# Performance work log

Measured on AMD Instinct MI355X. Metric: run time of the kernel, lower is better.

Reference implementation:

```python
import jax, jax.numpy as jnp
import numpy as np
import math

NUM_HEADS = 12
HEAD_DIM = 64
DEGREE = 3
POLY_DIM = HEAD_DIM * (DEGREE + 1)  # 256
MEM_HID = 512
HIDDEN = 768


def setup_inputs() -> dict:
    key = jax.random.key(0)
    ks = jax.random.split(key, 6)
    B, S = 4, 2048
    hidden_states = jax.random.normal(ks[0], (B, S, HIDDEN), dtype=jnp.float32)
    # q projection weight stored (in, out) so y = x @ Wq
    Wq = jax.random.normal(ks[1], (HIDDEN, HIDDEN), dtype=jnp.float32) / np.sqrt(HIDDEN)
    # polynomial coefficients initialized to 1/i!
    coeffs = jnp.array([1.0 / math.factorial(i) for i in range(DEGREE + 1)], dtype=jnp.float32)
    # deep memory MLP: Linear(poly_dim->mem_hid) + ReLU + Linear(mem_hid->poly_dim)
    W1 = jax.random.normal(ks[2], (POLY_DIM, MEM_HID), dtype=jnp.float32) / np.sqrt(POLY_DIM)
    b1 = jnp.zeros((MEM_HID,), dtype=jnp.float32)
    W2 = jax.random.normal(ks[3], (MEM_HID, POLY_DIM), dtype=jnp.float32) / np.sqrt(MEM_HID)
    b2 = jnp.zeros((POLY_DIM,), dtype=jnp.float32)
    return {"hidden_states": hidden_states, "Wq": Wq, "coeffs": coeffs,
            "W1": W1, "b1": b1, "W2": W2, "b2": b2}


def _poly_map(x, coeffs):
    # x: [..., head_dim] -> [..., head_dim*(degree+1)]
    xs = jnp.clip(x, -10.0, 10.0)
    feats = [coeffs[0] * jnp.ones_like(x)]
    for i in range(1, DEGREE + 1):
        feats.append(jnp.clip(coeffs[i] * xs ** i, -1e6, 1e6))
    return jnp.concatenate(feats, axis=-1)


def reference(hidden_states, Wq, coeffs, W1, b1, W2, b2):
    B, S, H = hidden_states.shape
    # q projection -> [B, S, nh, hd]
    q = (hidden_states @ Wq).reshape(B, S, NUM_HEADS, HEAD_DIM)
    # polynomial feature expansion -> [B, S, nh, poly_dim]
    poly_q = _poly_map(q, coeffs)
    flat = poly_q.reshape(-1, POLY_DIM)  # [B*S*nh, poly_dim]
    # deep memory MLP (test-time memory read)
    h = jax.nn.relu(flat @ W1 + b1)
    mem = h @ W2 + b2  # [B*S*nh, poly_dim]
    # slice first head_dim dims, fold heads back into hidden
    out = mem[:, :HEAD_DIM].reshape(B, S, NUM_HEADS * HEAD_DIM)
    return out
```

## Files before the change

### kernel.cpp

```cpp
#include <hip/hip_runtime.h>


typedef unsigned short u16;
typedef __attribute__((ext_vector_type(8))) short short8;
typedef __attribute__((ext_vector_type(4))) float f32x4;
typedef __attribute__((ext_vector_type(4))) u16 u16x4;

__device__ __forceinline__ u16 f2bf(float f) {
    unsigned u = __builtin_bit_cast(unsigned, f);
    u += 0x7FFFu + ((u >> 16) & 1u);
    return (u16)(u >> 16);
}

__device__ __forceinline__ unsigned cvtpk_bf16(float lo, float hi) {
    unsigned r;
    asm("v_cvt_pk_bf16_f32 %0, %1, %2" : "=v"(r) : "v"(lo), "v"(hi));
    return r;
}

__device__ __forceinline__ void gl2lds16(const void* g, void* l) {
    __builtin_amdgcn_global_load_lds(
        (const __attribute__((address_space(1))) unsigned int*)g,
        (__attribute__((address_space(3))) unsigned int*)l, 16, 0, 0);
}


__global__ __launch_bounds__(256) void cast_f32_bf16(const float* __restrict__ in,
                                                     u16* __restrict__ out, int n4) {
    int i = blockIdx.x * 256 + threadIdx.x;
    if (i < n4) {
        float4 v = reinterpret_cast<const float4*>(in)[i];
        u16x4 o = {f2bf(v.x), f2bf(v.y), f2bf(v.z), f2bf(v.w)};
        reinterpret_cast<u16x4*>(out)[i] = o;
    }
}

__global__ __launch_bounds__(256) void transpose_cast(const float* __restrict__ in,
                                                      u16* __restrict__ out,
                                                      int R, int Cin) {
    __shared__ float t[32][33];
    const int c0 = blockIdx.x * 32, r0 = blockIdx.y * 32;
    const int tx = threadIdx.x, ty = threadIdx.y;
    #pragma unroll
    for (int j = 0; j < 32; j += 8)
        t[ty + j][tx] = in[(size_t)(r0 + ty + j) * Cin + c0 + tx];
    __syncthreads();
    #pragma unroll
    for (int j = 0; j < 32; j += 8)
        out[(size_t)(c0 + ty + j) * R + r0 + tx] = f2bf(t[tx][ty + j]);
}

__global__ __launch_bounds__(256) void make_b1eff(const float* __restrict__ W1,
                                                  const float* __restrict__ b1,
                                                  const float* __restrict__ coeffs,
                                                  float* __restrict__ b1e) {
    const int n = blockIdx.x * 256 + threadIdx.x;
    float s = 0.f;
    #pragma unroll 8
    for (int k = 0; k < 64; ++k) s += W1[k * 512 + n];
    b1e[n] = b1[n] + coeffs[0] * s;
}


__global__ __launch_bounds__(256)
void gemm1_poly(const u16* __restrict__ A, const u16* __restrict__ B,
                const float* __restrict__ coeffs, u16* __restrict__ P)
{
    __shared__ u16 As[128 * 32];
    __shared__ u16 Bs[128 * 32];

    const int tid = threadIdx.x;
    const int w = tid >> 6, lane = tid & 63;
    const int lrow = lane >> 2, lslot = lane & 3;
    const int m16 = lane & 15, quad = lane >> 4;
    const int bm = blockIdx.x * 128, bn = blockIdx.y * 128;
    const int wr = (w & 1) * 64, wc = (w >> 1) * 64;

    const float c1 = coeffs[1], c2 = coeffs[2], c3 = coeffs[3];

    f32x4 acc[4][4];
    #pragma unroll
    for (int i = 0; i < 4; ++i)
        #pragma unroll
        for (int j = 0; j < 4; ++j)
            acc[i][j] = (f32x4){0.f, 0.f, 0.f, 0.f};

    for (int k0 = 0; k0 < 768; k0 += 32) {
        #pragma unroll
        for (int i = 0; i < 2; ++i) {
            const int row = (w * 2 + i) * 16 + lrow;
            const int cc = lslot ^ ((row >> 2) & 3);
            gl2lds16(A + (size_t)(bm + row) * 768 + k0 + cc * 8, &As[row * 32 + lslot * 8]);
            gl2lds16(B + (size_t)(bn + row) * 768 + k0 + cc * 8, &Bs[row * 32 + lslot * 8]);
        }
        __syncthreads();

        short8 af[4], bf[4];
        #pragma unroll
        for (int i = 0; i < 4; ++i) {
            const int row = wr + i * 16 + m16;
            const int s = quad ^ ((row >> 2) & 3);
            af[i] = *reinterpret_cast<const short8*>(&As[row * 32 + s * 8]);
        }
        #pragma unroll
        for (int j = 0; j < 4; ++j) {
            const int row = wc + j * 16 + m16;
            const int s = quad ^ ((row >> 2) & 3);
            bf[j] = *reinterpret_cast<const short8*>(&Bs[row * 32 + s * 8]);
        }
        #pragma unroll
        for (int i = 0; i < 4; ++i)
            #pragma unroll
            for (int j = 0; j < 4; ++j)
                acc[i][j] = __builtin_amdgcn_mfma_f32_16x16x32_bf16(af[i], bf[j], acc[i][j], 0, 0, 0);
        __syncthreads();
    }

    #pragma unroll
    for (int j = 0; j < 4; ++j) {
        const int col = bn + wc + j * 16 + m16;
        const int h = col >> 6, d = col & 63;
        #pragma unroll
        for (int i = 0; i < 4; ++i) {
            #pragma unroll
            for (int r = 0; r < 4; ++r) {
                const int row = bm + wr + i * 16 + quad * 4 + r;
                u16* pp = P + ((size_t)row * 12 + h) * 192 + d;
                float x = fminf(fmaxf(acc[i][j][r], -10.f), 10.f);
                const float x2 = x * x;
                const unsigned p12 = cvtpk_bf16(c1 * x, c2 * x2);
                const unsigned p3  = cvtpk_bf16(c3 * x2 * x, 0.f);
                pp[0]   = (u16)p12;
                pp[64]  = (u16)(p12 >> 16);
                pp[128] = (u16)p3;
            }
        }
    }
}

__global__ __launch_bounds__(256)
void gemm23(const u16* __restrict__ P, const u16* __restrict__ W1t,
            const float* __restrict__ b1e, const u16* __restrict__ W2t,
            const float* __restrict__ b2, float* __restrict__ out)
{
    __shared__ u16 As[128 * 32];
    __shared__ u16 Bs[128 * 32];
    __shared__ u16 Hs[4][128 * 32];

    const int tid = threadIdx.x;
    const int w = tid >> 6, lane = tid & 63;
    const int lrow = lane >> 2, lslot = lane & 3;
    const int m16 = lane & 15, quad = lane >> 4;
    const size_t r0 = (size_t)blockIdx.x * 128;
    const int w0 = w & 1, w1 = w >> 1;

    f32x4 accO[4][2];
    #pragma unroll
    for (int i = 0; i < 4; ++i)
        #pragma unroll
        for (int j = 0; j < 2; ++j)
            accO[i][j] = (f32x4){0.f, 0.f, 0.f, 0.f};

    #pragma unroll 1
    for (int s = 0; s < 4; ++s) {
        f32x4 accH[4][4];
        #pragma unroll
        for (int i = 0; i < 4; ++i)
            #pragma unroll
            for (int j = 0; j < 4; ++j)
                accH[i][j] = (f32x4){0.f, 0.f, 0.f, 0.f};

        for (int c = 0; c < 6; ++c) {
            #pragma unroll
            for (int i = 0; i < 2; ++i) {
                const int row = (w * 2 + i) * 16 + lrow;
                const int cc = lslot ^ ((row >> 2) & 3);
                gl2lds16(W1t + (size_t)(s * 128 + row) * 256 + 64 + c * 32 + cc * 8,
                         &As[row * 32 + lslot * 8]);
                gl2lds16(P + (r0 + row) * 192 + c * 32 + cc * 8,
                         &Bs[row * 32 + lslot * 8]);
            }
            __syncthreads();

            short8 af[4], bf[4];
            #pragma unroll
            for (int i = 0; i < 4; ++i) {
                const int row = w0 * 64 + i * 16 + m16;
                const int ss = quad ^ ((row >> 2) & 3);
                af[i] = *reinterpret_cast<const short8*>(&As[row * 32 + ss * 8]);
            }
            #pragma unroll
            for (int j = 0; j < 4; ++j) {
                const int row = w1 * 64 + j * 16 + m16;
                const int ss = quad ^ ((row >> 2) & 3);
                bf[j] = *reinterpret_cast<const short8*>(&Bs[row * 32 + ss * 8]);
            }
            #pragma unroll
            for (int i = 0; i < 4; ++i)
                #pragma unroll
                for (int j = 0; j < 4; ++j)
                    accH[i][j] = __builtin_amdgcn_mfma_f32_16x16x32_bf16(af[i], bf[j], accH[i][j], 0, 0, 0);
            __syncthreads();
        }

        #pragma unroll
        for (int i = 0; i < 4; ++i) {
            const int lb = w0 * 64 + i * 16 + quad * 4;
            const f32x4 bv = *reinterpret_cast<const f32x4*>(&b1e[s * 128 + lb]);
            const int hc = lb >> 5;
            #pragma unroll
            for (int j = 0; j < 4; ++j) {
                const int tc = w1 * 64 + j * 16 + m16;
                const float h0 = fmaxf(accH[i][j][0] + bv[0], 0.f);
                const float h1 = fmaxf(accH[i][j][1] + bv[1], 0.f);
                const float h2 = fmaxf(accH[i][j][2] + bv[2], 0.f);
                const float h3 = fmaxf(accH[i][j][3] + bv[3], 0.f);
                uint2 v;
                v.x = cvtpk_bf16(h0, h1);
                v.y = cvtpk_bf16(h2, h3);
                const int sl = ((lb >> 3) & 3) ^ ((tc >> 2) & 3);
                *reinterpret_cast<uint2*>(&Hs[hc][tc * 32 + sl * 8 + (lb & 7)]) = v;
            }
        }

        {
            u16* dst = (w < 2) ? As : Bs;
            #pragma unroll
            for (int i = 0; i < 4; ++i) {
                const int row = i * 16 + lrow;
                const int cc = lslot ^ ((row >> 2) & 3);
                gl2lds16(W2t + (size_t)row * 512 + s * 128 + w * 32 + cc * 8,
                         dst + (w & 1) * 2048 + row * 32 + lslot * 8);
            }
        }
        __syncthreads();

        #pragma unroll
        for (int c = 0; c < 4; ++c) {
            short8 a3[4], b3[2];
            #pragma unroll
            for (int i = 0; i < 4; ++i) {
                const int tr = w0 * 64 + i * 16 + m16;
                const int ss = quad ^ ((tr >> 2) & 3);
                a3[i] = *reinterpret_cast<const short8*>(&Hs[c][tr * 32 + ss * 8]);
            }
            const u16* wsrc = ((c < 2) ? (const u16*)As : (const u16*)Bs) + (c & 1) * 2048;
            #pragma unroll
            for (int j = 0; j < 2; ++j) {
                const int rowb = w1 * 32 + j * 16 + m16;
                const int ss = quad ^ ((rowb >> 2) & 3);
                b3[j] = *reinterpret_cast<const short8*>(wsrc + rowb * 32 + ss * 8);
            }
            #pragma unroll
            for (int i = 0; i < 4; ++i)
                #pragma unroll
                for (int j = 0; j < 2; ++j)
                    accO[i][j] = __builtin_amdgcn_mfma_f32_16x16x32_bf16(a3[i], b3[j], accO[i][j], 0, 0, 0);
        }
        __syncthreads();
    }

    #pragma unroll
    for (int j = 0; j < 2; ++j) {
        const int col = w1 * 32 + j * 16 + m16;
        const float bv = b2[col];
        #pragma unroll
        for (int i = 0; i < 4; ++i) {
            #pragma unroll
            for (int r = 0; r < 4; ++r) {
                const int row = w0 * 64 + i * 16 + quad * 4 + r;
                out[(r0 + row) * 64 + col] = accO[i][j][r] + bv;
            }
        }
    }
}


extern "C" void kernel_launch(void* const* d_in, const int* in_sizes, int n_in,
                              void* d_out, int out_size, void* d_ws, size_t ws_size,
                              hipStream_t stream) {
    const float* X      = (const float*)d_in[0];
    const float* Wq     = (const float*)d_in[1];
    const float* coeffs = (const float*)d_in[2];
    const float* W1     = (const float*)d_in[3];
    const float* b1     = (const float*)d_in[4];
    const float* W2     = (const float*)d_in[5];
    const float* b2     = (const float*)d_in[6];

    char* ws = (char*)d_ws;
    u16*   Xb  = (u16*)(ws);
    u16*   Wqb = (u16*)(ws + 12582912);
    u16*   W1b = (u16*)(ws + 13762560);
    u16*   W2b = (u16*)(ws + 14024704);
    float* b1e = (float*)(ws + 14090240);
    u16*   P   = (u16*)(ws + 14092288);

    cast_f32_bf16<<<6144, 256, 0, stream>>>(X, Xb, 8192 * 768 / 4);
    transpose_cast<<<dim3(24, 24), dim3(32, 8), 0, stream>>>(Wq, Wqb, 768, 768);
    transpose_cast<<<dim3(16, 8),  dim3(32, 8), 0, stream>>>(W1, W1b, 256, 512);
    transpose_cast<<<dim3(2, 16),  dim3(32, 8), 0, stream>>>(W2, W2b, 512, 256);
    make_b1eff<<<2, 256, 0, stream>>>(W1, b1, coeffs, b1e);

    gemm1_poly<<<dim3(64, 6), 256, 0, stream>>>(Xb, Wqb, coeffs, P);

    gemm23<<<dim3(768), 256, 0, stream>>>(P, W1b, b1e, W2b, b2, (float*)d_out);
}
```

Before: 178.1 us.

## Restructure both GEMM kernels: double-buffer gemm1, stage poly output, shrink gemm23 tiles

gemm1_poly now uses 64-token tiles with double-buffered LDS staging, and writes its polynomial features through LDS so the global stores to P are coalesced 16-byte vectors instead of scattered 2-byte writes. gemm23 halves its row tile to 64, preloads the whole P tile into LDS once, and reads W1 and W2 fragments straight from global/L2 into registers with software prefetch. This drops most per-k barriers and adds launch_bounds occupancy 3 with twice as many blocks. The cost is more redundant weight reads from global memory and less reuse per tile.

After: 227.0 us. 27.5% more time.

```diff
diff --git a/kernel.cpp b/kernel.cpp
--- a/kernel.cpp
+++ b/kernel.cpp
@@ -63,145 +63,187 @@
 
 
 __global__ __launch_bounds__(256)
-void gemm1_poly(const u16* __restrict__ A, const u16* __restrict__ B,
+void gemm1_poly(const u16* __restrict__ Xb, const u16* __restrict__ Wqb,
                 const float* __restrict__ coeffs, u16* __restrict__ P)
 {
-    __shared__ u16 As[128 * 32];
-    __shared__ u16 Bs[128 * 32];
+    __shared__ u16 lds[128 * 200];
 
     const int tid = threadIdx.x;
     const int w = tid >> 6, lane = tid & 63;
     const int lrow = lane >> 2, lslot = lane & 3;
     const int m16 = lane & 15, quad = lane >> 4;
-    const int bm = blockIdx.x * 128, bn = blockIdx.y * 128;
-    const int wr = (w & 1) * 64, wc = (w >> 1) * 64;
+    const int w0 = w & 1, w1 = w >> 1;
+    const int tok0 = blockIdx.x * 64;
+    const int bn = blockIdx.y * 128;
+    const int h0 = blockIdx.y * 2;
 
     const float c1 = coeffs[1], c2 = coeffs[2], c3 = coeffs[3];
 
-    f32x4 acc[4][4];
+    f32x4 acc[4][2];
     #pragma unroll
     for (int i = 0; i < 4; ++i)
         #pragma unroll
-        for (int j = 0; j < 4; ++j)
+        for (int j = 0; j < 2; ++j)
             acc[i][j] = (f32x4){0.f, 0.f, 0.f, 0.f};
 
-    for (int k0 = 0; k0 < 768; k0 += 32) {
+    auto stage = [&](int buf, int k0) {
+        u16* Xs = lds + buf * 6144;
+        u16* Ws = Xs + 2048;
+        {
+            const int row = w * 16 + lrow;
+            const int cc = lslot ^ ((row >> 2) & 3);
+            gl2lds16(Xb + (size_t)(tok0 + row) * 768 + k0 + cc * 8, &Xs[row * 32 + lslot * 8]);
+        }
         #pragma unroll
         for (int i = 0; i < 2; ++i) {
             const int row = (w * 2 + i) * 16 + lrow;
             const int cc = lslot ^ ((row >> 2) & 3);
-            gl2lds16(A + (size_t)(bm + row) * 768 + k0 + cc * 8, &As[row * 32 + lslot * 8]);
-            gl2lds16(B + (size_t)(bn + row) * 768 + k0 + cc * 8, &Bs[row * 32 + lslot * 8]);
-        }
+            gl2lds16(Wqb + (size_t)(bn + row) * 768 + k0 + cc * 8, &Ws[row * 32 + lslot * 8]);
+        }
+    };
+
+    stage(0, 0);
+    __syncthreads();
+    int cur = 0;
+
+    for (int k0 = 0; k0 < 768; k0 += 32) {
+        if (k0 + 32 < 768) stage(cur ^ 1, k0 + 32);
+        const u16* Xs = lds + cur * 6144;
+        const u16* Ws = Xs + 2048;
+        short8 a[4], b[2];
+        #pragma unroll
+        for (int i = 0; i < 4; ++i) {
+            const int row = w0 * 64 + i * 16 + m16;
+            const int ss = quad ^ ((row >> 2) & 3);
+            a[i] = *reinterpret_cast<const short8*>(&Ws[row * 32 + ss * 8]);
+        }
+        #pragma unroll
+        for (int j = 0; j < 2; ++j) {
+            const int row = w1 * 32 + j * 16 + m16;
+            const int ss = quad ^ ((row >> 2) & 3);
+            b[j] = *reinterpret_cast<const short8*>(&Xs[row * 32 + ss * 8]);
+        }
+        #pragma unroll
+        for (int i = 0; i < 4; ++i)
+            #pragma unroll
+            for (int j = 0; j < 2; ++j)
+                acc[i][j] = __builtin_amdgcn_mfma_f32_16x16x32_bf16(a[i], b[j], acc[i][j], 0, 0, 0);
         __syncthreads();
-
-        short8 af[4], bf[4];
-        #pragma unroll
-        for (int i = 0; i < 4; ++i) {
-            const int row = wr + i * 16 + m16;
-            const int s = quad ^ ((row >> 2) & 3);
-            af[i] = *reinterpret_cast<const short8*>(&As[row * 32 + s * 8]);
-        }
-        #pragma unroll
-        for (int j = 0; j < 4; ++j) {
-            const int row = wc + j * 16 + m16;
-            const int s = quad ^ ((row >> 2) & 3);
-            bf[j] = *reinterpret_cast<const short8*>(&Bs[row * 32 + s * 8]);
-        }
-        #pragma unroll
-        for (int i = 0; i < 4; ++i)
-            #pragma unroll
-            for (int j = 0; j < 4; ++j)
-                acc[i][j] = __builtin_amdgcn_mfma_f32_16x16x32_bf16(af[i], bf[j], acc[i][j], 0, 0, 0);
-        __syncthreads();
-    }
-
-    #pragma unroll
-    for (int j = 0; j < 4; ++j) {
-        const int col = bn + wc + j * 16 + m16;
-        const int h = col >> 6, d = col & 63;
-        #pragma unroll
-        for (int i = 0; i < 4; ++i) {
+        cur ^= 1;
+    }
+
+    #pragma unroll
+    for (int i = 0; i < 4; ++i) {
+        const int d0 = i * 16 + quad * 4;
+        #pragma unroll
+        for (int j = 0; j < 2; ++j) {
+            const int tokLocal = w1 * 32 + j * 16 + m16;
+            u16* base = &lds[(tokLocal * 2 + w0) * 200 + d0];
+            float x[4], x2[4];
             #pragma unroll
             for (int r = 0; r < 4; ++r) {
-                const int row = bm + wr + i * 16 + quad * 4 + r;
-                u16* pp = P + ((size_t)row * 12 + h) * 192 + d;
-                float x = fminf(fmaxf(acc[i][j][r], -10.f), 10.f);
-                const float x2 = x * x;
-                const unsigned p12 = cvtpk_bf16(c1 * x, c2 * x2);
-                const unsigned p3  = cvtpk_bf16(c3 * x2 * x, 0.f);
-                pp[0]   = (u16)p12;
-                pp[64]  = (u16)(p12 >> 16);
-                pp[128] = (u16)p3;
-            }
-        }
-    }
-}
-
-__global__ __launch_bounds__(256)
+                x[r] = fminf(fmaxf(acc[i][j][r], -10.f), 10.f);
+                x2[r] = x[r] * x[r];
+            }
+            uint2 p1, p2, p3;
+            p1.x = cvtpk_bf16(c1 * x[0], c1 * x[1]);
+            p1.y = cvtpk_bf16(c1 * x[2], c1 * x[3]);
+            p2.x = cvtpk_bf16(c2 * x2[0], c2 * x2[1]);
+            p2.y = cvtpk_bf16(c2 * x2[2], c2 * x2[3]);
+            p3.x = cvtpk_bf16(c3 * x2[0] * x[0], c3 * x2[1] * x[1]);
+            p3.y = cvtpk_bf16(c3 * x2[2] * x[2], c3 * x2[3] * x[3]);
+            *reinterpret_cast<uint2*>(base)       = p1;
+            *reinterpret_cast<uint2*>(base + 64)  = p2;
+            *reinterpret_cast<uint2*>(base + 128) = p3;
+        }
+    }
+    __syncthreads();
+
+    #pragma unroll
+    for (int ii = 0; ii < 12; ++ii) {
+        const int flat = ii * 256 + tid;
+        const int rowL = flat / 24, ck = flat % 24;
+        const int tokL = rowL >> 1, hh = rowL & 1;
+        const size_t prow = ((size_t)(tok0 + tokL) * 12 + h0 + hh);
+        short8 v = *reinterpret_cast<const short8*>(&lds[rowL * 200 + ck * 8]);
+        *reinterpret_cast<short8*>(P + prow * 192 + ck * 8) = v;
+    }
+}
+
+
+__global__ __launch_bounds__(256, 3)
 void gemm23(const u16* __restrict__ P, const u16* __restrict__ W1t,
             const float* __restrict__ b1e, const u16* __restrict__ W2t,
             const float* __restrict__ b2, float* __restrict__ out)
 {
-    __shared__ u16 As[128 * 32];
-    __shared__ u16 Bs[128 * 32];
-    __shared__ u16 Hs[4][128 * 32];
+    __shared__ u16 Ps[6][64 * 32];
+    __shared__ u16 Hs[4][64 * 32];
 
     const int tid = threadIdx.x;
     const int w = tid >> 6, lane = tid & 63;
     const int lrow = lane >> 2, lslot = lane & 3;
     const int m16 = lane & 15, quad = lane >> 4;
-    const size_t r0 = (size_t)blockIdx.x * 128;
+    const size_t r0 = (size_t)blockIdx.x * 64;
     const int w0 = w & 1, w1 = w >> 1;
 
-    f32x4 accO[4][2];
-    #pragma unroll
-    for (int i = 0; i < 4; ++i)
+    #pragma unroll
+    for (int c = 0; c < 6; ++c) {
+        const int row = w * 16 + lrow;
+        const int cc = lslot ^ ((row >> 2) & 3);
+        gl2lds16(P + (r0 + row) * 192 + c * 32 + cc * 8, &Ps[c][row * 32 + lslot * 8]);
+    }
+
+    f32x4 accO[2][2];
+    #pragma unroll
+    for (int i = 0; i < 2; ++i)
         #pragma unroll
         for (int j = 0; j < 2; ++j)
             accO[i][j] = (f32x4){0.f, 0.f, 0.f, 0.f};
 
+    __syncthreads();
+
     #pragma unroll 1
     for (int s = 0; s < 4; ++s) {
-        f32x4 accH[4][4];
+        f32x4 accH[4][2];
         #pragma unroll
         for (int i = 0; i < 4; ++i)
             #pragma unroll
-            for (int j = 0; j < 4; ++j)
+            for (int j = 0; j < 2; ++j)
                 accH[i][j] = (f32x4){0.f, 0.f, 0.f, 0.f};
 
+        short8 afn[4];
+        #pragma unroll
+        for (int i = 0; i < 4; ++i)
+            afn[i] = *reinterpret_cast<const short8*>(
+                W1t + (size_t)(s * 128 + w0 * 64 + i * 16 + m16) * 256 + 64 + quad * 8);
+
+        #pragma unroll
         for (int c = 0; c < 6; ++c) {
-            #pragma unroll
-            for (int i = 0; i < 2; ++i) {
-                const int row = (w * 2 + i) * 16 + lrow;
-                const int cc = lslot ^ ((row >> 2) & 3);
-                gl2lds16(W1t + (size_t)(s * 128 + row) * 256 + 64 + c * 32 + cc * 8,
-                         &As[row * 32 + lslot * 8]);
-                gl2lds16(P + (r0 + row) * 192 + c * 32 + cc * 8,
-                         &Bs[row * 32 + lslot * 8]);
-            }
-            __syncthreads();
-
-            short8 af[4], bf[4];
-            #pragma unroll
-            for (int i = 0; i < 4; ++i) {
-                const int row = w0 * 64 + i * 16 + m16;
+            short8 af[4];
+            #pragma unroll
+            for (int i = 0; i < 4; ++i) af[i] = afn[i];
+            if (c < 5) {
+                #pragma unroll
+                for (int i = 0; i < 4; ++i)
+                    afn[i] = *reinterpret_cast<const short8*>(
+                        W1t + (size_t)(s * 128 + w0 * 64 + i * 16 + m16) * 256
+                            + 64 + (c + 1) * 32 + quad * 8);
+            }
+            short8 bf[2];
+            #pragma unroll
+            for (int j = 0; j < 2; ++j) {
+                const int row = w1 * 32 + j * 16 + m16;
                 const int ss = quad ^ ((row >> 2) & 3);
-                af[i] = *reinterpret_cast<const short8*>(&As[row * 32 + ss * 8]);
-            }
-            #pragma unroll
-            for (int j = 0; j < 4; ++j) {
-                const int row = w1 * 64 + j * 16 + m16;
-                const int ss = quad ^ ((row >> 2) & 3);
-                bf[j] = *reinterpret_cast<const short8*>(&Bs[row * 32 + ss * 8]);
+                bf[j] = *reinterpret_cast<const short8*>(&Ps[c][row * 32 + ss * 8]);
             }
             #pragma unroll
             for (int i = 0; i < 4; ++i)
                 #pragma unroll
-                for (int j = 0; j < 4; ++j)
+                for (int j = 0; j < 2; ++j)
                     accH[i][j] = __builtin_amdgcn_mfma_f32_16x16x32_bf16(af[i], bf[j], accH[i][j], 0, 0, 0);
-            __syncthreads();
-        }
+        }
+
+        __syncthreads();
 
         #pragma unroll
         for (int i = 0; i < 4; ++i) {
@@ -209,55 +251,41 @@
             const f32x4 bv = *reinterpret_cast<const f32x4*>(&b1e[s * 128 + lb]);
             const int hc = lb >> 5;
             #pragma unroll
-            for (int j = 0; j < 4; ++j) {
-                const int tc = w1 * 64 + j * 16 + m16;
-                const float h0 = fmaxf(accH[i][j][0] + bv[0], 0.f);
-                const float h1 = fmaxf(accH[i][j][1] + bv[1], 0.f);
-                const float h2 = fmaxf(accH[i][j][2] + bv[2], 0.f);
-                const float h3 = fmaxf(accH[i][j][3] + bv[3], 0.f);
+            for (int j = 0; j < 2; ++j) {
+                const int tc = w1 * 32 + j * 16 + m16;
+                const float h0v = fmaxf(accH[i][j][0] + bv[0], 0.f);
+                const float h1v = fmaxf(accH[i][j][1] + bv[1], 0.f);
+                const float h2v = fmaxf(accH[i][j][2] + bv[2], 0.f);
+                const float h3v = fmaxf(accH[i][j][3] + bv[3], 0.f);
                 uint2 v;
-                v.x = cvtpk_bf16(h0, h1);
-                v.y = cvtpk_bf16(h2, h3);
+                v.x = cvtpk_bf16(h0v, h1v);
+                v.y = cvtpk_bf16(h2v, h3v);
                 const int sl = ((lb >> 3) & 3) ^ ((tc >> 2) & 3);
                 *reinterpret_cast<uint2*>(&Hs[hc][tc * 32 + sl * 8 + (lb & 7)]) = v;
             }
         }
 
-        {
-            u16* dst = (w < 2) ? As : Bs;
-            #pragma unroll
-            for (int i = 0; i < 4; ++i) {
-                const int row = i * 16 + lrow;
-                const int cc = lslot ^ ((row >> 2) & 3);
-                gl2lds16(W2t + (size_t)row * 512 + s * 128 + w * 32 + cc * 8,
-                         dst + (w & 1) * 2048 + row * 32 + lslot * 8);
-            }
-        }
         __syncthreads();
 
         #pragma unroll
         for (int c = 0; c < 4; ++c) {
-            short8 a3[4], b3[2];
-            #pragma unroll
-            for (int i = 0; i < 4; ++i) {
-                const int tr = w0 * 64 + i * 16 + m16;
+            short8 a3[2], b3[2];
+            #pragma unroll
+            for (int i = 0; i < 2; ++i) {
+                const int tr = w0 * 32 + i * 16 + m16;
                 const int ss = quad ^ ((tr >> 2) & 3);
                 a3[i] = *reinterpret_cast<const short8*>(&Hs[c][tr * 32 + ss * 8]);
             }
-            const u16* wsrc = ((c < 2) ? (const u16*)As : (const u16*)Bs) + (c & 1) * 2048;
-            #pragma unroll
-            for (int j = 0; j < 2; ++j) {
-                const int rowb = w1 * 32 + j * 16 + m16;
-                const int ss = quad ^ ((rowb >> 2) & 3);
-                b3[j] = *reinterpret_cast<const short8*>(wsrc + rowb * 32 + ss * 8);
-            }
-            #pragma unroll
-            for (int i = 0; i < 4; ++i)
+            #pragma unroll
+            for (int j = 0; j < 2; ++j)
+                b3[j] = *reinterpret_cast<const short8*>(
+                    W2t + (size_t)(w1 * 32 + j * 16 + m16) * 512 + s * 128 + c * 32 + quad * 8);
+            #pragma unroll
+            for (int i = 0; i < 2; ++i)
                 #pragma unroll
                 for (int j = 0; j < 2; ++j)
                     accO[i][j] = __builtin_amdgcn_mfma_f32_16x16x32_bf16(a3[i], b3[j], accO[i][j], 0, 0, 0);
         }
-        __syncthreads();
     }
 
     #pragma unroll
@@ -265,10 +293,10 @@
         const int col = w1 * 32 + j * 16 + m16;
         const float bv = b2[col];
         #pragma unroll
-        for (int i = 0; i < 4; ++i) {
+        for (int i = 0; i < 2; ++i) {
             #pragma unroll
             for (int r = 0; r < 4; ++r) {
-                const int row = w0 * 64 + i * 16 + quad * 4 + r;
+                const int row = w0 * 32 + i * 16 + quad * 4 + r;
                 out[(r0 + row) * 64 + col] = accO[i][j][r] + bv;
             }
         }
@@ -301,7 +329,7 @@
     transpose_cast<<<dim3(2, 16),  dim3(32, 8), 0, stream>>>(W2, W2b, 512, 256);
     make_b1eff<<<2, 256, 0, stream>>>(W1, b1, coeffs, b1e);
 
-    gemm1_poly<<<dim3(64, 6), 256, 0, stream>>>(Xb, Wqb, coeffs, P);
-
-    gemm23<<<dim3(768), 256, 0, stream>>>(P, W1b, b1e, W2b, b2, (float*)d_out);
-}
+    gemm1_poly<<<dim3(128, 6), 256, 0, stream>>>(Xb, Wqb, coeffs, P);
+
+    gemm23<<<dim3(1536), 256, 0, stream>>>(P, W1b, b1e, W2b, b2, (float*)d_out);
+}
```
